# Kernel tuning notes

Measured on AMD Instinct MI355X. Metric: run time of the kernel, lower is better.

Reference implementation:

```python
import jax, jax.numpy as jnp
import numpy as np
from jax import lax

ALPHA = 0.3
BETA = 0.1


def setup_inputs() -> dict:
    key = jax.random.key(0)
    x = jax.random.normal(key, (32, 4096, 512), dtype=jnp.float32)
    return {"x": x}


def _dema(x):
    # x: [B, T, F]
    alpha = jnp.asarray(ALPHA, dtype=x.dtype)
    beta = jnp.asarray(BETA, dtype=x.dtype)
    s0 = x[:, 0, :]                 # [B, F] level init
    b0 = x[:, 1, :] - s0            # [B, F] trend init

    def step(carry, xt):
        s_prev, b = carry
        s = alpha * xt + (1 - alpha) * (s_prev + b)
        b_new = beta * (s - s_prev) + (1 - beta) * b
        return (s, b_new), s

    xs = jnp.moveaxis(x[:, 1:, :], 1, 0)      # [T-1, B, F]
    _, ss = lax.scan(step, (s0, b0), xs)      # ss: [T-1, B, F]
    out = jnp.concatenate([s0[:, None, :], jnp.moveaxis(ss, 0, 1)], axis=1)
    return out                                # [B, T, F]


def reference(x) -> jnp.ndarray:
    return _dema(x)
```

## Files before the change

### kernel.cpp

```cpp
#include <hip/hip_runtime.h>


#define DEMA_ALPHA 0.3f
#define DEMA_BETA  0.1f
#define DEMA_T     4096
#define DEMA_B     32
#define DEMA_F     512
#define DEMA_F4    (DEMA_F / 4)
#define DEMA_L     64
#define DEMA_H     96
#define DEMA_C     (DEMA_T / DEMA_L)

__device__ __forceinline__ void dema_step(float4& s, float4& bb, const float4 xt) {
    const float a  = DEMA_ALPHA;
    const float a1 = 1.0f - DEMA_ALPHA;
    const float be = DEMA_BETA;
    const float b1 = 1.0f - DEMA_BETA;
    float4 sp = s;
    s.x = a * xt.x + a1 * (sp.x + bb.x);
    s.y = a * xt.y + a1 * (sp.y + bb.y);
    s.z = a * xt.z + a1 * (sp.z + bb.z);
    s.w = a * xt.w + a1 * (sp.w + bb.w);
    bb.x = be * (s.x - sp.x) + b1 * bb.x;
    bb.y = be * (s.y - sp.y) + b1 * bb.y;
    bb.z = be * (s.z - sp.z) + b1 * bb.z;
    bb.w = be * (s.w - sp.w) + b1 * bb.w;
}

__global__ __launch_bounds__(128, 4) void dema_kernel(const float* __restrict__ x,
                                                      float* __restrict__ out) {
    const int f4 = threadIdx.x;
    const int b  = blockIdx.x;
    const int c  = blockIdx.y;

    const float4* __restrict__ xp =
        reinterpret_cast<const float4*>(x) + (size_t)b * DEMA_T * DEMA_F4 + f4;
    float4* __restrict__ op =
        reinterpret_cast<float4*>(out) + (size_t)b * DEMA_T * DEMA_F4 + f4;

    const int t0 = c * DEMA_L;
    float4 s, bb;
    int t;

    if (t0 <= DEMA_H) {
        s = xp[0];
        float4 x1 = xp[DEMA_F4];
        bb.x = x1.x - s.x;
        bb.y = x1.y - s.y;
        bb.z = x1.z - s.z;
        bb.w = x1.w - s.w;
        if (c == 0) op[0] = s;
        t = 1;
    } else {
        const int tw = t0 - DEMA_H;
        s = xp[(tw - 1) * DEMA_F4];
        float4 x1 = xp[tw * DEMA_F4];
        bb.x = x1.x - s.x;
        bb.y = x1.y - s.y;
        bb.z = x1.z - s.z;
        bb.w = x1.w - s.w;
        t = tw;
    }

    #pragma unroll 4
    for (; t < t0; ++t) {
        dema_step(s, bb, xp[t * DEMA_F4]);
    }
    const int tend = t0 + DEMA_L;
    #pragma unroll 4
    for (; t < tend; ++t) {
        dema_step(s, bb, xp[t * DEMA_F4]);
        op[t * DEMA_F4] = s;
    }
}

extern "C" void kernel_launch(void* const* d_in, const int* in_sizes, int n_in,
                              void* d_out, int out_size, void* d_ws, size_t ws_size,
                              hipStream_t stream) {
    const float* x = (const float*)d_in[0];
    float* out = (float*)d_out;

    dim3 block(128, 1, 1);
    dim3 grid(DEMA_B, DEMA_C, 1);
    dema_kernel<<<grid, block, 0, stream>>>(x, out);
}
```

Measured before the change: 509.9 us.

## Software-pipeline DEMA scan with register ring buffer and longer chunks

Each block now handles 256 timesteps after a 128-step warmup, up from 64 timesteps after a 96-step warmup, so redundant warmup reads per output drop sharply. The recurrence is fed from a 16-deep register ring buffer. Loads are issued with inline asm global_load_dwordx4, and explicit s_waitcnt vmcnt fences plus scheduling barriers keep about 16 loads in flight ahead of the serial dependency chain. The trade-off is far fewer blocks (occupancy hint dropped to 1) and hand-tuned wait counts that depend on how stores are counted in vmcnt.

```diff
diff --git a/kernel.cpp b/kernel.cpp
--- a/kernel.cpp
+++ b/kernel.cpp
@@ -5,72 +5,126 @@
 #define DEMA_BETA  0.1f
 #define DEMA_T     4096
 #define DEMA_B     32
-#define DEMA_F     512
-#define DEMA_F4    (DEMA_F / 4)
-#define DEMA_L     64
-#define DEMA_H     96
+#define DEMA_F4    128
+#define DEMA_L     256
+#define DEMA_H     128
 #define DEMA_C     (DEMA_T / DEMA_L)
+#define SD         16
 
-__device__ __forceinline__ void dema_step(float4& s, float4& bb, const float4 xt) {
-    const float a  = DEMA_ALPHA;
-    const float a1 = 1.0f - DEMA_ALPHA;
-    const float be = DEMA_BETA;
-    const float b1 = 1.0f - DEMA_BETA;
-    float4 sp = s;
-    s.x = a * xt.x + a1 * (sp.x + bb.x);
-    s.y = a * xt.y + a1 * (sp.y + bb.y);
-    s.z = a * xt.z + a1 * (sp.z + bb.z);
-    s.w = a * xt.w + a1 * (sp.w + bb.w);
-    bb.x = be * (s.x - sp.x) + b1 * bb.x;
-    bb.y = be * (s.y - sp.y) + b1 * bb.y;
-    bb.z = be * (s.z - sp.z) + b1 * bb.z;
-    bb.w = be * (s.w - sp.w) + b1 * bb.w;
+typedef float v4f __attribute__((ext_vector_type(4)));
+
+#define SB() __builtin_amdgcn_sched_barrier(0)
+#define WAIT15() asm volatile("s_waitcnt vmcnt(15)")
+#define WAIT30() asm volatile("s_waitcnt vmcnt(30)")
+#define ASM_LOAD(dst, ptr) \
+    asm volatile("global_load_dwordx4 %0, %1, off" : "=v"(dst) : "v"(ptr) : "memory")
+
+__device__ __forceinline__ void dema_step(v4f& s, v4f& bb, const v4f xt) {
+    const v4f sp = s;
+    s  = DEMA_ALPHA * xt + (1.0f - DEMA_ALPHA) * (sp + bb);
+    bb = DEMA_BETA * (s - sp) + (1.0f - DEMA_BETA) * bb;
 }
 
-__global__ __launch_bounds__(128, 4) void dema_kernel(const float* __restrict__ x,
+__global__ __launch_bounds__(128, 1) void dema_kernel(const float* __restrict__ x,
                                                       float* __restrict__ out) {
     const int f4 = threadIdx.x;
     const int b  = blockIdx.x;
     const int c  = blockIdx.y;
 
-    const float4* __restrict__ xp =
-        reinterpret_cast<const float4*>(x) + (size_t)b * DEMA_T * DEMA_F4 + f4;
-    float4* __restrict__ op =
-        reinterpret_cast<float4*>(out) + (size_t)b * DEMA_T * DEMA_F4 + f4;
+    const v4f* __restrict__ xp =
+        reinterpret_cast<const v4f*>(x) + (size_t)b * DEMA_T * DEMA_F4 + f4;
+    v4f* __restrict__ op =
+        reinterpret_cast<v4f*>(out) + (size_t)b * DEMA_T * DEMA_F4 + f4;
 
-    const int t0 = c * DEMA_L;
-    float4 s, bb;
-    int t;
+    v4f buf[SD];
+    v4f s, bb;
 
-    if (t0 <= DEMA_H) {
-        s = xp[0];
-        float4 x1 = xp[DEMA_F4];
-        bb.x = x1.x - s.x;
-        bb.y = x1.y - s.y;
-        bb.z = x1.z - s.z;
-        bb.w = x1.w - s.w;
-        if (c == 0) op[0] = s;
-        t = 1;
+    if (c == 0) {
+        v4f x0 = xp[0];
+        v4f x1 = xp[DEMA_F4];
+        s = x0; bb = x1 - x0;
+        op[0] = s;
+        #pragma unroll
+        for (int j = 0; j < SD; ++j)
+            ASM_LOAD(buf[j], xp + (size_t)(1 + j) * DEMA_F4);
+        #pragma unroll
+        for (int j = 0; j < SD; ++j) {
+            WAIT15(); SB();
+            dema_step(s, bb, buf[j]);
+            op[(size_t)(1 + j) * DEMA_F4] = s;
+            ASM_LOAD(buf[j], xp + (size_t)(17 + j) * DEMA_F4);
+        }
+        #pragma unroll 1
+        for (int g = 1; g < 14; ++g) {
+            #pragma unroll
+            for (int j = 0; j < SD; ++j) {
+                const int r = 1 + 16 * g + j;
+                WAIT30(); SB();
+                dema_step(s, bb, buf[j]);
+                op[(size_t)r * DEMA_F4] = s;
+                ASM_LOAD(buf[j], xp + (size_t)(r + 16) * DEMA_F4);
+            }
+        }
+        #pragma unroll
+        for (int j = 0; j < SD; ++j) {
+            const int r = 225 + j;
+            WAIT30(); SB();
+            dema_step(s, bb, buf[j]);
+            op[(size_t)r * DEMA_F4] = s;
+            if (j < 15) ASM_LOAD(buf[j], xp + (size_t)(r + 16) * DEMA_F4);
+        }
+        #pragma unroll
+        for (int j = 0; j < 15; ++j) {
+            const int r = 241 + j;
+            WAIT15(); SB();
+            dema_step(s, bb, buf[j]);
+            op[(size_t)r * DEMA_F4] = s;
+        }
     } else {
+        const int t0 = c * DEMA_L;
         const int tw = t0 - DEMA_H;
-        s = xp[(tw - 1) * DEMA_F4];
-        float4 x1 = xp[tw * DEMA_F4];
-        bb.x = x1.x - s.x;
-        bb.y = x1.y - s.y;
-        bb.z = x1.z - s.z;
-        bb.w = x1.w - s.w;
-        t = tw;
-    }
+        const v4f* __restrict__ xw = xp + (size_t)tw * DEMA_F4;
+        v4f* __restrict__ ow = op + (size_t)tw * DEMA_F4;
 
-    #pragma unroll 4
-    for (; t < t0; ++t) {
-        dema_step(s, bb, xp[t * DEMA_F4]);
-    }
-    const int tend = t0 + DEMA_L;
-    #pragma unroll 4
-    for (; t < tend; ++t) {
-        dema_step(s, bb, xp[t * DEMA_F4]);
-        op[t * DEMA_F4] = s;
+        v4f sm1 = xw[-DEMA_F4];
+        v4f x0  = xw[0];
+        s = sm1; bb = x0 - sm1;
+        #pragma unroll
+        for (int j = 0; j < SD; ++j)
+            ASM_LOAD(buf[j], xw + (size_t)j * DEMA_F4);
+        #pragma unroll 1
+        for (int g = 0; g < 8; ++g) {
+            #pragma unroll
+            for (int j = 0; j < SD; ++j) {
+                WAIT15(); SB();
+                dema_step(s, bb, buf[j]);
+                ASM_LOAD(buf[j], xw + (size_t)(16 * g + j + 16) * DEMA_F4);
+            }
+        }
+        #pragma unroll
+        for (int j = 0; j < SD; ++j) {
+            WAIT15(); SB();
+            dema_step(s, bb, buf[j]);
+            ow[(size_t)(128 + j) * DEMA_F4] = s;
+            ASM_LOAD(buf[j], xw + (size_t)(144 + j) * DEMA_F4);
+        }
+        #pragma unroll 1
+        for (int g = 1; g < 15; ++g) {
+            #pragma unroll
+            for (int j = 0; j < SD; ++j) {
+                const int r = 128 + 16 * g + j;
+                WAIT30(); SB();
+                dema_step(s, bb, buf[j]);
+                ow[(size_t)r * DEMA_F4] = s;
+                ASM_LOAD(buf[j], xw + (size_t)(r + 16) * DEMA_F4);
+            }
+        }
+        #pragma unroll
+        for (int j = 0; j < SD; ++j) {
+            WAIT15(); SB();
+            dema_step(s, bb, buf[j]);
+            ow[(size_t)(368 + j) * DEMA_F4] = s;
+        }
     }
 }
 
```

Measured after the change: 477.3 us. 1.07x faster.
